# Performance work log

Hardware: AMD Instinct MI355X
Metric: run time of the kernel (lower is better)

The kernel has to match this reference:

```python
import jax, jax.numpy as jnp
import numpy as np

B = 2
H = W = 128
N = H * W            # 16384 nodes
K_LOC = 7 * 7        # 49 local neighbors (KxK unfold window)
K_LONG = int(K_LOC * 0.2)  # 9 long-range random neighbors
KT = K_LOC + K_LONG  # 58 total neighbors per node
D = 64               # prop_dim
EPS = 1e-12


def setup_inputs() -> dict:
    key = jax.random.key(0)
    k1, k2, k3 = jax.random.split(key, 3)
    logits = jax.random.normal(k1, (B, N, KT), dtype=jnp.float32)
    h0 = jax.random.normal(k2, (B, N, D), dtype=jnp.float32)
    v_inds = jax.random.randint(k3, (B, N, KT), 0, N)  # neighbor (column) indices
    return {"logits": logits, "h0": h0, "v_inds": v_inds, "num_iters": 10}


def reference(logits, h0, v_inds, num_iters):
    """Core of SymbolicGrouper.extract_segments:
    - local adjacency: softmax over K then max-normalize per row
    - scatter into (transposed) sparse global affinity: A[v, u] = adj[u, k], v = v_inds[u, k]
    - graph propagation: h <- normalize(A @ h), iterated.
    """
    Bn, Nn, Kt = logits.shape
    # local adjacency: softmax + max-normalize (matches extract_segments)
    adj = jax.nn.softmax(logits, axis=-1)
    adj = adj / jnp.clip(jnp.max(adj, axis=-1, keepdims=True), EPS, None)
    # validity mask (col_inds < N in local_to_sparse_global_affinity)
    adj = jnp.where(v_inds < Nn, adj, jnp.zeros((), adj.dtype))
    # h0 initialized as softmax of normal noise
    h = jax.nn.softmax(h0, axis=-1)

    def prop_one(adj_b, v_b, h_b):
        v_flat = v_b.reshape(-1)  # [N*K]

        def step(hc, _):
            # message from source node u along each of its K edges: [N, K, D]
            contrib = adj_b[:, :, None] * hc[:, None, :]
            # transposed scatter: accumulate into destination v (A^T semantics)
            out = jnp.zeros_like(hc).at[v_flat].add(contrib.reshape(-1, hc.shape[-1]))
            # per-node L2 renormalization keeps propagation stable
            out = out / jnp.clip(jnp.linalg.norm(out, axis=-1, keepdims=True), EPS, None)
            return out, None

        h_final, _ = jax.lax.scan(step, h_b, None, length=num_iters)
        return h_final

    return jax.vmap(prop_one)(adj, v_inds, h)  # [B, N, D]
```

## Files before the change

kernel.cpp:

```cpp
#include <hip/hip_runtime.h>
#include <hip/hip_fp16.h>

#define B_ 2
#define N_ 16384
#define KT_ 58
#define D_ 64
#define BN_ (B_ * N_)
#define EDGES_ (B_ * N_ * KT_)
#define NUM_ITERS_ 10
#define EPS_ 1e-12f
#define CAP_ 128
#define NPART_ 8
#define FBLK_ 256
#define CHUNK_ (EDGES_ / FBLK_)

__global__ __launch_bounds__(256) void k_adj(const float* __restrict__ logits,
                                             const int* __restrict__ v_inds,
                                             unsigned int* __restrict__ packed) {
    const int lane = threadIdx.x & 63;
    const int r = blockIdx.x * 4 + (threadIdx.x >> 6);
    float l = (lane < KT_) ? logits[(size_t)r * KT_ + lane] : -INFINITY;
    float m = l;
    #pragma unroll
    for (int off = 32; off; off >>= 1) m = fmaxf(m, __shfl_xor(m, off));
    if (lane < KT_) {
        const int v = v_inds[(size_t)r * KT_ + lane];
        float w = (v < N_) ? __expf(l - m) : 0.f;
        unsigned int wb = (unsigned int)__half_as_ushort(__float2half_rn(w));
        unsigned int vv = (v < N_) ? (unsigned int)v : 0u;
        packed[(size_t)r * KT_ + lane] = (wb << 16) | vv;
    }
}

__global__ __launch_bounds__(256) void k_fillx(const unsigned int* __restrict__ packed,
                                               int* __restrict__ cursor,
                                               unsigned int* __restrict__ bucket) {
    const int part = blockIdx.x & (NPART_ - 1);
    const int m = blockIdx.x >> 3;
    const int t = threadIdx.x;
    const int base = m * CHUNK_;
    #pragma unroll 4
    for (int i = 0; i < CHUNK_ / 256; ++i) {
        const int e = base + i * 256 + t;
        const unsigned int pk = __builtin_nontemporal_load(packed + e);
        const int v = (int)(pk & 0x3fffu);
        const int gv = ((e >= N_ * KT_) ? N_ : 0) + v;
        if ((gv >> 12) == part) {
            const unsigned int u = (unsigned int)(e / KT_);
            const int pos = atomicAdd(&cursor[gv], 1);
            if (pos < CAP_) bucket[(size_t)gv * CAP_ + pos] = (pk & 0xffff0000u) | u;
        }
    }
}

__global__ __launch_bounds__(256) void k_hinit(const float* __restrict__ h0,
                                               __half* __restrict__ h) {
    const int lane = threadIdx.x & 63;
    const int r = blockIdx.x * 4 + (threadIdx.x >> 6);
    float x = h0[(size_t)r * D_ + lane];
    float m = x;
    #pragma unroll
    for (int off = 32; off; off >>= 1) m = fmaxf(m, __shfl_xor(m, off));
    float ex = __expf(x - m);
    float s = ex;
    #pragma unroll
    for (int off = 32; off; off >>= 1) s += __shfl_xor(s, off);
    h[(size_t)r * D_ + lane] = __float2half_rn(ex / s);
}

#define PROC_EDGE(REC, A0, A1, A2, A3, A4, A5, A6, A7)                        \
    {                                                                          \
        const float w =                                                        \
            __half2float(__ushort_as_half((unsigned short)((REC) >> 16)));     \
        const int u = (int)((REC) & 0xffffu);                                  \
        const uint4 x = h4[(size_t)u * 8 + j];                                 \
        const __half2 p0 = *(const __half2*)&x.x;                              \
        const __half2 p1 = *(const __half2*)&x.y;                              \
        const __half2 p2 = *(const __half2*)&x.z;                              \
        const __half2 p3 = *(const __half2*)&x.w;                              \
        A0 = fmaf(__half2float(__low2half(p0)), w, A0);                        \
        A1 = fmaf(__half2float(__high2half(p0)), w, A1);                       \
        A2 = fmaf(__half2float(__low2half(p1)), w, A2);                        \
        A3 = fmaf(__half2float(__high2half(p1)), w, A3);                       \
        A4 = fmaf(__half2float(__low2half(p2)), w, A4);                        \
        A5 = fmaf(__half2float(__high2half(p2)), w, A5);                       \
        A6 = fmaf(__half2float(__low2half(p3)), w, A6);                        \
        A7 = fmaf(__half2float(__high2half(p3)), w, A7);                       \
    }

template <bool FINAL>
__global__ __launch_bounds__(256) void k_prop(const int* __restrict__ cursor,
                                              const unsigned int* __restrict__ bucket,
                                              const __half* __restrict__ h_in,
                                              __half* __restrict__ h_out,
                                              float* __restrict__ out_f) {
    const int lane = threadIdx.x & 63;
    const int grp = lane >> 3;
    const int j = lane & 7;
    const int p = blockIdx.x & 7;
    const int m = blockIdx.x >> 3;
    const int wid = threadIdx.x >> 6;
    int g0 = (p << 12) + (((m << 2) + wid) << 1);
    g0 = __builtin_amdgcn_readfirstlane(g0);
    const int g1 = g0 + 1;

    const int cntA = min(cursor[g0], CAP_);
    const int cntB = min(cursor[g1], CAP_);
    const unsigned int* browA = bucket + (size_t)g0 * CAP_;
    const unsigned int* browB = bucket + (size_t)g1 * CAP_;
    const unsigned int r0A = browA[lane];
    const unsigned int r0B = browB[lane];
    const uint4* __restrict__ h4 = (const uint4*)h_in;

    float a0 = 0.f, a1 = 0.f, a2 = 0.f, a3 = 0.f;
    float a4 = 0.f, a5 = 0.f, a6 = 0.f, a7 = 0.f;
    float b0 = 0.f, b1 = 0.f, b2 = 0.f, b3 = 0.f;
    float b4 = 0.f, b5 = 0.f, b6 = 0.f, b7 = 0.f;

    #pragma unroll 4
    for (int e0 = 0; e0 < 64; e0 += 8) {
        const int e = e0 + grp;
        unsigned int recA = __shfl(r0A, e);
        unsigned int recB = __shfl(r0B, e);
        recA = (e < cntA) ? recA : 0u;
        recB = (e < cntB) ? recB : 0u;
        PROC_EDGE(recA, a0, a1, a2, a3, a4, a5, a6, a7)
        PROC_EDGE(recB, b0, b1, b2, b3, b4, b5, b6, b7)
    }
    if (cntA > 64) {
        const unsigned int r1A = browA[64 + lane];
        for (int e0 = 64; e0 < cntA; e0 += 8) {
            const int e = e0 + grp;
            unsigned int rec = __shfl(r1A, e & 63);
            rec = (e < cntA) ? rec : 0u;
            PROC_EDGE(rec, a0, a1, a2, a3, a4, a5, a6, a7)
        }
    }
    if (cntB > 64) {
        const unsigned int r1B = browB[64 + lane];
        for (int e0 = 64; e0 < cntB; e0 += 8) {
            const int e = e0 + grp;
            unsigned int rec = __shfl(r1B, e & 63);
            rec = (e < cntB) ? rec : 0u;
            PROC_EDGE(rec, b0, b1, b2, b3, b4, b5, b6, b7)
        }
    }

    #pragma unroll
    for (int off = 8; off <= 32; off <<= 1) {
        a0 += __shfl_xor(a0, off); a1 += __shfl_xor(a1, off);
        a2 += __shfl_xor(a2, off); a3 += __shfl_xor(a3, off);
        a4 += __shfl_xor(a4, off); a5 += __shfl_xor(a5, off);
        a6 += __shfl_xor(a6, off); a7 += __shfl_xor(a7, off);
        b0 += __shfl_xor(b0, off); b1 += __shfl_xor(b1, off);
        b2 += __shfl_xor(b2, off); b3 += __shfl_xor(b3, off);
        b4 += __shfl_xor(b4, off); b5 += __shfl_xor(b5, off);
        b6 += __shfl_xor(b6, off); b7 += __shfl_xor(b7, off);
    }

    float nA = a0 * a0 + a1 * a1 + a2 * a2 + a3 * a3 +
               a4 * a4 + a5 * a5 + a6 * a6 + a7 * a7;
    float nB = b0 * b0 + b1 * b1 + b2 * b2 + b3 * b3 +
               b4 * b4 + b5 * b5 + b6 * b6 + b7 * b7;
    #pragma unroll
    for (int off = 4; off; off >>= 1) {
        nA += __shfl_xor(nA, off);
        nB += __shfl_xor(nB, off);
    }
    const float invA = 1.0f / fmaxf(sqrtf(nA), EPS_);
    const float invB = 1.0f / fmaxf(sqrtf(nB), EPS_);

    if (grp == 0) {
        if (FINAL) {
            float4* oA = (float4*)out_f + (size_t)g0 * 16 + j * 2;
            oA[0] = make_float4(a0 * invA, a1 * invA, a2 * invA, a3 * invA);
            oA[1] = make_float4(a4 * invA, a5 * invA, a6 * invA, a7 * invA);
            float4* oB = (float4*)out_f + (size_t)g1 * 16 + j * 2;
            oB[0] = make_float4(b0 * invB, b1 * invB, b2 * invB, b3 * invB);
            oB[1] = make_float4(b4 * invB, b5 * invB, b6 * invB, b7 * invB);
        } else {
            __half2 q0 = __floats2half2_rn(a0 * invA, a1 * invA);
            __half2 q1 = __floats2half2_rn(a2 * invA, a3 * invA);
            __half2 q2 = __floats2half2_rn(a4 * invA, a5 * invA);
            __half2 q3 = __floats2half2_rn(a6 * invA, a7 * invA);
            uint4 oA;
            oA.x = *(const unsigned int*)&q0;
            oA.y = *(const unsigned int*)&q1;
            oA.z = *(const unsigned int*)&q2;
            oA.w = *(const unsigned int*)&q3;
            ((uint4*)h_out)[(size_t)g0 * 8 + j] = oA;
            __half2 s0 = __floats2half2_rn(b0 * invB, b1 * invB);
            __half2 s1 = __floats2half2_rn(b2 * invB, b3 * invB);
            __half2 s2 = __floats2half2_rn(b4 * invB, b5 * invB);
            __half2 s3 = __floats2half2_rn(b6 * invB, b7 * invB);
            uint4 oB;
            oB.x = *(const unsigned int*)&s0;
            oB.y = *(const unsigned int*)&s1;
            oB.z = *(const unsigned int*)&s2;
            oB.w = *(const unsigned int*)&s3;
            ((uint4*)h_out)[(size_t)g1 * 8 + j] = oB;
        }
    }
}

extern "C" void kernel_launch(void* const* d_in, const int* in_sizes, int n_in,
                              void* d_out, int out_size, void* d_ws, size_t ws_size,
                              hipStream_t stream) {
    const float* logits = (const float*)d_in[0];
    const float* h0 = (const float*)d_in[1];
    const int* v_inds = (const int*)d_in[2];
    float* out = (float*)d_out;

    char* ws = (char*)d_ws;
    size_t off = 0;
    auto alloc = [&](size_t bytes) {
        void* p = ws + off;
        off = (off + bytes + 255) & ~(size_t)255;
        return p;
    };
    unsigned int* packed = (unsigned int*)alloc((size_t)EDGES_ * 4);
    unsigned int* bucket = (unsigned int*)alloc((size_t)BN_ * CAP_ * 4);
    int* cursor   = (int*)alloc((size_t)BN_ * 4);
    __half* h_a   = (__half*)alloc((size_t)BN_ * D_ * 2);
    __half* h_b   = (__half*)alloc((size_t)BN_ * D_ * 2);

    hipMemsetAsync(cursor, 0, (size_t)BN_ * 4, stream);

    k_adj<<<BN_ / 4, 256, 0, stream>>>(logits, v_inds, packed);
    k_hinit<<<BN_ / 4, 256, 0, stream>>>(h0, h_a);
    k_fillx<<<NPART_ * FBLK_, 256, 0, stream>>>(packed, cursor, bucket);

    const __half* cur = h_a;
    for (int i = 0; i < NUM_ITERS_; ++i) {
        __half* nxt = (i & 1) ? h_a : h_b;
        if (i == NUM_ITERS_ - 1) {
            k_prop<true><<<BN_ / 8, 256, 0, stream>>>(cursor, bucket, cur, nullptr, out);
        } else {
            k_prop<false><<<BN_ / 8, 256, 0, stream>>>(cursor, bucket, cur, nxt, nullptr);
        }
        cur = nxt;
    }
}
```

Before: 381.4 us.

## Replace global-atomic bucket fill with two-pass LDS binning and mixed-precision FMA

Replaces the partitioned global-atomic scatter that builds per-node edge buckets with a two-pass scheme. The first kernel bins edges into 256 coarse bins using LDS counters and one global atomic per bin per block. The second kernel assembles per-row buckets in LDS and writes them out densely, zero-padding unused slots. This removes per-edge global atomics and the cursor memset, and it lets the propagation loop drop its per-edge bounds masks because empty slots now hold zero records. It also adds inline v_fma_mix_f32 assembly to fuse the fp16 unpack with the FMA, but it caps rows at 112 edges and bins at 8192 entries, so overflow edges are silently dropped.

```diff
diff --git a/kernel.cpp b/kernel.cpp
--- a/kernel.cpp
+++ b/kernel.cpp
@@ -10,9 +10,11 @@
 #define NUM_ITERS_ 10
 #define EPS_ 1e-12f
 #define CAP_ 128
-#define NPART_ 8
-#define FBLK_ 256
-#define CHUNK_ (EDGES_ / FBLK_)
+#define LCAP_ 112
+#define NBIN_ 256
+#define BINSZ_ 8192
+#define P1BLK_ 256
+#define P1CHUNK_ (EDGES_ / P1BLK_)
 
 __global__ __launch_bounds__(256) void k_adj(const float* __restrict__ logits,
                                              const int* __restrict__ v_inds,
@@ -32,25 +34,70 @@
     }
 }
 
-__global__ __launch_bounds__(256) void k_fillx(const unsigned int* __restrict__ packed,
-                                               int* __restrict__ cursor,
-                                               unsigned int* __restrict__ bucket) {
-    const int part = blockIdx.x & (NPART_ - 1);
-    const int m = blockIdx.x >> 3;
+__global__ __launch_bounds__(256) void k_bin(const unsigned int* __restrict__ packed,
+                                             int* __restrict__ gBinCnt,
+                                             unsigned int* __restrict__ binRec,
+                                             unsigned char* __restrict__ binRow) {
+    __shared__ int cnt[NBIN_];
+    __shared__ int base[NBIN_];
+    __shared__ int cur[NBIN_];
     const int t = threadIdx.x;
-    const int base = m * CHUNK_;
+    cnt[t] = 0;
+    __syncthreads();
+    const int e0 = blockIdx.x * P1CHUNK_;
     #pragma unroll 4
-    for (int i = 0; i < CHUNK_ / 256; ++i) {
-        const int e = base + i * 256 + t;
-        const unsigned int pk = __builtin_nontemporal_load(packed + e);
-        const int v = (int)(pk & 0x3fffu);
-        const int gv = ((e >= N_ * KT_) ? N_ : 0) + v;
-        if ((gv >> 12) == part) {
-            const unsigned int u = (unsigned int)(e / KT_);
-            const int pos = atomicAdd(&cursor[gv], 1);
-            if (pos < CAP_) bucket[(size_t)gv * CAP_ + pos] = (pk & 0xffff0000u) | u;
-        }
-    }
+    for (int i = 0; i < P1CHUNK_ / 256; ++i) {
+        const int e = e0 + i * 256 + t;
+        const unsigned int pk = packed[e];
+        const int gv = ((e >= N_ * KT_) ? N_ : 0) + (int)(pk & 0x3fffu);
+        atomicAdd(&cnt[gv >> 7], 1);
+    }
+    __syncthreads();
+    base[t] = atomicAdd(&gBinCnt[t], cnt[t]);
+    cur[t] = 0;
+    __syncthreads();
+    #pragma unroll 4
+    for (int i = 0; i < P1CHUNK_ / 256; ++i) {
+        const int e = e0 + i * 256 + t;
+        const unsigned int pk = packed[e];
+        const int gv = ((e >= N_ * KT_) ? N_ : 0) + (int)(pk & 0x3fffu);
+        const int bin = gv >> 7;
+        const unsigned int u = (unsigned int)(e / KT_);
+        const int slot = atomicAdd(&cur[bin], 1);
+        const int pos = base[bin] + slot;
+        if (pos < BINSZ_) {
+            binRec[((size_t)bin << 13) + pos] = (pk & 0xffff0000u) | u;
+            binRow[((size_t)bin << 13) + pos] = (unsigned char)(gv & 127);
+        }
+    }
+}
+
+__global__ __launch_bounds__(256) void k_bucket(const int* __restrict__ gBinCnt,
+                                                const unsigned int* __restrict__ binRec,
+                                                const unsigned char* __restrict__ binRow,
+                                                unsigned int* __restrict__ bucket,
+                                                int* __restrict__ dcnt) {
+    __shared__ unsigned int rows[128 * LCAP_];
+    __shared__ int rcnt[128];
+    const int t = threadIdx.x;
+    for (int i = t; i < 128 * LCAP_; i += 256) rows[i] = 0;
+    if (t < 128) rcnt[t] = 0;
+    __syncthreads();
+    const int b = blockIdx.x;
+    const int n = min(gBinCnt[b], BINSZ_);
+    for (int i = t; i < n; i += 256) {
+        const unsigned int rec = binRec[((size_t)b << 13) + i];
+        const int row = (int)binRow[((size_t)b << 13) + i];
+        const int slot = atomicAdd(&rcnt[row], 1);
+        if (slot < LCAP_) rows[row * LCAP_ + slot] = rec;
+    }
+    __syncthreads();
+    for (int i = t; i < 128 * CAP_; i += 256) {
+        const int row = i >> 7, slot = i & 127;
+        const unsigned int val = (slot < LCAP_) ? rows[row * LCAP_ + slot] : 0u;
+        bucket[(((size_t)b << 7) + row) * CAP_ + slot] = val;
+    }
+    if (t < 128) dcnt[(b << 7) + t] = min(rcnt[t], LCAP_);
 }
 
 __global__ __launch_bounds__(256) void k_hinit(const float* __restrict__ h0,
@@ -68,28 +115,27 @@
     h[(size_t)r * D_ + lane] = __float2half_rn(ex / s);
 }
 
+#define FMA_MIX(ACC, PK, REC, SEL0)                                            \
+    asm("v_fma_mix_f32 %0, %1, %2, %0 op_sel:[" SEL0 ",1,0] op_sel_hi:[1,1,0]" \
+        : "+v"(ACC)                                                            \
+        : "v"(PK), "v"(REC));
+
 #define PROC_EDGE(REC, A0, A1, A2, A3, A4, A5, A6, A7)                        \
     {                                                                          \
-        const float w =                                                        \
-            __half2float(__ushort_as_half((unsigned short)((REC) >> 16)));     \
         const int u = (int)((REC) & 0xffffu);                                  \
         const uint4 x = h4[(size_t)u * 8 + j];                                 \
-        const __half2 p0 = *(const __half2*)&x.x;                              \
-        const __half2 p1 = *(const __half2*)&x.y;                              \
-        const __half2 p2 = *(const __half2*)&x.z;                              \
-        const __half2 p3 = *(const __half2*)&x.w;                              \
-        A0 = fmaf(__half2float(__low2half(p0)), w, A0);                        \
-        A1 = fmaf(__half2float(__high2half(p0)), w, A1);                       \
-        A2 = fmaf(__half2float(__low2half(p1)), w, A2);                        \
-        A3 = fmaf(__half2float(__high2half(p1)), w, A3);                       \
-        A4 = fmaf(__half2float(__low2half(p2)), w, A4);                        \
-        A5 = fmaf(__half2float(__high2half(p2)), w, A5);                       \
-        A6 = fmaf(__half2float(__low2half(p3)), w, A6);                        \
-        A7 = fmaf(__half2float(__high2half(p3)), w, A7);                       \
+        FMA_MIX(A0, x.x, (REC), "0")                                           \
+        FMA_MIX(A1, x.x, (REC), "1")                                           \
+        FMA_MIX(A2, x.y, (REC), "0")                                           \
+        FMA_MIX(A3, x.y, (REC), "1")                                           \
+        FMA_MIX(A4, x.z, (REC), "0")                                           \
+        FMA_MIX(A5, x.z, (REC), "1")                                           \
+        FMA_MIX(A6, x.w, (REC), "0")                                           \
+        FMA_MIX(A7, x.w, (REC), "1")                                           \
     }
 
 template <bool FINAL>
-__global__ __launch_bounds__(256) void k_prop(const int* __restrict__ cursor,
+__global__ __launch_bounds__(256) void k_prop(const int* __restrict__ dcnt,
                                               const unsigned int* __restrict__ bucket,
                                               const __half* __restrict__ h_in,
                                               __half* __restrict__ h_out,
@@ -104,8 +150,8 @@
     g0 = __builtin_amdgcn_readfirstlane(g0);
     const int g1 = g0 + 1;
 
-    const int cntA = min(cursor[g0], CAP_);
-    const int cntB = min(cursor[g1], CAP_);
+    const int cntA = dcnt[g0];
+    const int cntB = dcnt[g1];
     const unsigned int* browA = bucket + (size_t)g0 * CAP_;
     const unsigned int* browB = bucket + (size_t)g1 * CAP_;
     const unsigned int r0A = browA[lane];
@@ -120,10 +166,8 @@
     #pragma unroll 4
     for (int e0 = 0; e0 < 64; e0 += 8) {
         const int e = e0 + grp;
-        unsigned int recA = __shfl(r0A, e);
-        unsigned int recB = __shfl(r0B, e);
-        recA = (e < cntA) ? recA : 0u;
-        recB = (e < cntB) ? recB : 0u;
+        const unsigned int recA = __shfl(r0A, e);
+        const unsigned int recB = __shfl(r0B, e);
         PROC_EDGE(recA, a0, a1, a2, a3, a4, a5, a6, a7)
         PROC_EDGE(recB, b0, b1, b2, b3, b4, b5, b6, b7)
     }
@@ -218,25 +262,29 @@
         off = (off + bytes + 255) & ~(size_t)255;
         return p;
     };
-    unsigned int* packed = (unsigned int*)alloc((size_t)EDGES_ * 4);
     unsigned int* bucket = (unsigned int*)alloc((size_t)BN_ * CAP_ * 4);
-    int* cursor   = (int*)alloc((size_t)BN_ * 4);
-    __half* h_a   = (__half*)alloc((size_t)BN_ * D_ * 2);
-    __half* h_b   = (__half*)alloc((size_t)BN_ * D_ * 2);
-
-    hipMemsetAsync(cursor, 0, (size_t)BN_ * 4, stream);
+    unsigned int* packed = bucket;
+    unsigned int* binRec = (unsigned int*)alloc((size_t)NBIN_ * BINSZ_ * 4);
+    unsigned char* binRow = (unsigned char*)alloc((size_t)NBIN_ * BINSZ_);
+    int* gBinCnt = (int*)alloc((size_t)NBIN_ * 4);
+    int* dcnt    = (int*)alloc((size_t)BN_ * 4);
+    __half* h_a  = (__half*)alloc((size_t)BN_ * D_ * 2);
+    __half* h_b  = (__half*)alloc((size_t)BN_ * D_ * 2);
+
+    hipMemsetAsync(gBinCnt, 0, (size_t)NBIN_ * 4, stream);
 
     k_adj<<<BN_ / 4, 256, 0, stream>>>(logits, v_inds, packed);
     k_hinit<<<BN_ / 4, 256, 0, stream>>>(h0, h_a);
-    k_fillx<<<NPART_ * FBLK_, 256, 0, stream>>>(packed, cursor, bucket);
+    k_bin<<<P1BLK_, 256, 0, stream>>>(packed, gBinCnt, binRec, binRow);
+    k_bucket<<<NBIN_, 256, 0, stream>>>(gBinCnt, binRec, binRow, bucket, dcnt);
 
     const __half* cur = h_a;
     for (int i = 0; i < NUM_ITERS_; ++i) {
         __half* nxt = (i & 1) ? h_a : h_b;
         if (i == NUM_ITERS_ - 1) {
-            k_prop<true><<<BN_ / 8, 256, 0, stream>>>(cursor, bucket, cur, nullptr, out);
+            k_prop<true><<<BN_ / 8, 256, 0, stream>>>(dcnt, bucket, cur, nullptr, out);
         } else {
-            k_prop<false><<<BN_ / 8, 256, 0, stream>>>(cursor, bucket, cur, nxt, nullptr);
+            k_prop<false><<<BN_ / 8, 256, 0, stream>>>(dcnt, bucket, cur, nxt, nullptr);
         }
         cur = nxt;
     }
```

New measurement: 345.6 us. -9.4%, faster.
